# Performance work log

Hardware: AMD Instinct MI355X
Metric: run time of the kernel (lower is better)

## Reference

```python
import jax, jax.numpy as jnp
import numpy as np


def l2norm(x):
    return x / jnp.linalg.norm(x, axis=-1, keepdims=True)


def setup_inputs() -> dict:
    key = jax.random.key(0)
    ks = jax.random.split(key, 20)
    B, D, Wd, V, N, L = 384, 1024, 300, 30000, 8000, 16
    s = 1.0 / np.sqrt(D)
    inp = {
        "r": jax.random.normal(ks[0], (B, D), jnp.float32),
        "m": jax.random.normal(ks[1], (B, D), jnp.float32),
        "t": jax.random.normal(ks[2], (B, D), jnp.float32),
        "noun_token_id": jax.random.randint(ks[3], (B, L), 0, V, jnp.int32),
        "noun_len": jax.random.randint(ks[4], (B,), 1, L + 1, jnp.int32),
        "all_nouns_token": jax.random.randint(ks[5], (N,), 0, V, jnp.int32),
        "embed_table": jax.random.normal(ks[6], (V, Wd), jnp.float32) * 0.02,
        "noun_W": jax.random.normal(ks[7], (Wd, D), jnp.float32) / np.sqrt(Wd),
        "noun_b": jnp.zeros((D,), jnp.float32),
        "em_W1": jax.random.normal(ks[8], (D, D), jnp.float32) * s,
        "em_b1": jnp.zeros((D,), jnp.float32),
        "em_W2": jax.random.normal(ks[9], (D, D), jnp.float32) * s,
        "em_b2": jnp.zeros((D,), jnp.float32),
        "tr_W": jax.random.normal(ks[10], (D, D), jnp.float32) * s,
        "tr_b": jnp.zeros((D,), jnp.float32),
    }
    # dict noun_token_id_to_idx as dense map; 0 == missing (torch `if weight_idx:` falsy)
    idx = jax.random.randint(ks[11], (V,), 0, N, jnp.int32)
    present = jax.random.uniform(ks[12], (V,)) < 0.7
    inp["token_to_idx_map"] = jnp.where(present, idx, 0).astype(jnp.int32)
    return inp


def reference(r, m, t, noun_token_id, noun_len, all_nouns_token, token_to_idx_map,
              embed_table, noun_W, noun_b, em_W1, em_b1, em_W2, em_b2, tr_W, tr_b):
    B, D = m.shape
    L = noun_token_id.shape[1]

    # cls_weights = noun_encoder(embed(all_nouns_token))  -> [N, D]
    cls_weights = embed_table[all_nouns_token] @ noun_W + noun_b

    # gen_cpt: vectorized replacement of the per-token python double loop (@no_grad)
    widx = token_to_idx_map[noun_token_id]                # [B, L]
    found = widx > 0                                      # `if weight_idx:` semantics
    mapped = cls_weights[widx]                            # [B, L, D]
    fallback = embed_table[noun_token_id] @ noun_W + noun_b  # noun_encoder(embed(key))
    valid = jnp.arange(L)[None, :] < noun_len[:, None]    # [B, L]
    concepts = jnp.where((found & valid)[..., None], mapped,
                         jnp.where(valid[..., None], fallback, 0.0))
    concepts = jax.lax.stop_gradient(concepts)            # torch.no_grad

    # Attention_EM(m): Linear -> ReLU -> Linear -> Softmax(dim=1)
    h = jax.nn.relu(m @ em_W1 + em_b1)
    A_EM = jax.nn.softmax(h @ em_W2 + em_b2, axis=1)      # [B, D]
    Tr_m = l2norm(m @ tr_W + tr_b)                        # Transform_m

    # EM broadcast: (Tr_m[b] * l2norm(A_EM[b]*t[c])).sum(-1)
    # = ((Tr_m*A_EM)[b] . t[c]) / ||A_EM[b]*t[c]||, expressed as two GEMMs
    num = jnp.einsum('bd,cd->bc', Tr_m * A_EM, t)
    den = jnp.sqrt(jnp.einsum('bd,cd->bc', A_EM * A_EM, t * t))
    EM_score = num / den                                  # [B, B]

    # IS broadcast: cosine(r, t)
    IS_score = l2norm(r) @ l2norm(t).T                    # [B, B]

    score = EM_score + IS_score
    return score, concepts
```

## Files before the change

### kernel.cpp

```cpp
#include <hip/hip_runtime.h>
#include <hip/hip_bf16.h>

#define BDIM 384
#define DDIM 1024
#define LDIM 16
#define WD 300
#define CK 320
#define NROWS (BDIM * LDIM)
#define FELEM (BDIM * DDIM)
#define SELEM (BDIM * BDIM)

typedef __attribute__((ext_vector_type(8))) short short8v;
typedef _Float16 half8 __attribute__((ext_vector_type(8)));
typedef __attribute__((ext_vector_type(4))) float f32x4;

__device__ inline ushort f2bf(float x) {
    union { float f; unsigned u; } c; c.f = x;
    unsigned u = c.u;
    unsigned r = (u + 0x7fffu + ((u >> 16) & 1u)) >> 16;
    return (ushort)r;
}

#define PRE_A 1920
#define PRE_B (PRE_A + 320)
#define PRE_T (PRE_B + 3072)
#define PRE_M (PRE_T + 384)
__global__ __launch_bounds__(256) void prep_all(
    const float* __restrict__ embed, const int* __restrict__ ntid,
    const int* __restrict__ nlen, const int* __restrict__ ant, const int* __restrict__ t2i,
    ushort* __restrict__ Abf, int* __restrict__ rowtok,
    const float* __restrict__ nW, ushort* __restrict__ BbfT,
    const float* __restrict__ W1, const float* __restrict__ W2, const float* __restrict__ W3,
    _Float16* __restrict__ WT1, _Float16* __restrict__ WT2, _Float16* __restrict__ WT3,
    const float* __restrict__ m, _Float16* __restrict__ mh) {
    __shared__ float tile[32][33];
    const int b = blockIdx.x, t = threadIdx.x;

    if (b < PRE_A) {
        int idx = b * 256 + t;
        int row = idx / (CK / 4);
        int q = idx - row * (CK / 4);
        int tok = ntid[row];
        int w = t2i[tok];
        int eff = (w > 0) ? ant[w] : tok;
        bool valid = (row & 15) < nlen[row >> 4];
        if (q == 0) rowtok[row] = valid ? eff : -1;
        ushort4 o = {0, 0, 0, 0};
        if (valid && q < WD / 4) {
            float4 v = *(const float4*)&embed[(size_t)eff * WD + q * 4];
            o.x = f2bf(v.x); o.y = f2bf(v.y); o.z = f2bf(v.z); o.w = f2bf(v.w);
        }
        *(ushort4*)&Abf[(size_t)row * CK + q * 4] = o;
        return;
    }
    if (b < PRE_B) {
        int bb = b - PRE_A;
        const int k0 = (bb % 10) * 32, c0 = (bb / 10) * 32;
        const int r = t >> 3, q = t & 7;
        int k = k0 + r;
        float4 v = {0, 0, 0, 0};
        if (k < WD) v = *(const float4*)&nW[(size_t)k * DDIM + c0 + q * 4];
        tile[r][q * 4 + 0] = v.x; tile[r][q * 4 + 1] = v.y;
        tile[r][q * 4 + 2] = v.z; tile[r][q * 4 + 3] = v.w;
        __syncthreads();
        ushort4 o;
        o.x = f2bf(tile[q * 4 + 0][r]);
        o.y = f2bf(tile[q * 4 + 1][r]);
        o.z = f2bf(tile[q * 4 + 2][r]);
        o.w = f2bf(tile[q * 4 + 3][r]);
        *(ushort4*)&BbfT[(size_t)(c0 + r) * CK + k0 + q * 4] = o;
        return;
    }
    if (b < PRE_T) {
        int bb = b - PRE_B;
        int z = bb >> 10, rem = bb & 1023;
        const float* W = (z == 0) ? W1 : (z == 1) ? W2 : W3;
        _Float16* WT = (z == 0) ? WT1 : (z == 1) ? WT2 : WT3;
        const int k0 = (rem & 31) * 32, c0 = (rem >> 5) * 32;
        const int r = t >> 3, q = t & 7;
        float4 v = *(const float4*)&W[(size_t)(k0 + r) * DDIM + c0 + q * 4];
        tile[r][q * 4 + 0] = v.x; tile[r][q * 4 + 1] = v.y;
        tile[r][q * 4 + 2] = v.z; tile[r][q * 4 + 3] = v.w;
        __syncthreads();
        union { _Float16 h[4]; ushort4 u; } o;
        o.h[0] = (_Float16)tile[q * 4 + 0][r];
        o.h[1] = (_Float16)tile[q * 4 + 1][r];
        o.h[2] = (_Float16)tile[q * 4 + 2][r];
        o.h[3] = (_Float16)tile[q * 4 + 3][r];
        *(ushort4*)&WT[(size_t)(c0 + r) * DDIM + k0 + q * 4] = o.u;
        return;
    }
    {
        int bb = b - PRE_T;
        int i = bb * 1024 + t * 4;
        float4 v = *(const float4*)&m[i];
        union { _Float16 h[4]; ushort4 u; } o;
        o.h[0] = (_Float16)v.x; o.h[1] = (_Float16)v.y;
        o.h[2] = (_Float16)v.z; o.h[3] = (_Float16)v.w;
        *(ushort4*)&mh[i] = o.u;
    }
}

__global__ __launch_bounds__(256) void concepts_mfma(const ushort* __restrict__ Abf,
                                                     const ushort* __restrict__ BbfT,
                                                     const int* __restrict__ rowtok,
                                                     const float* __restrict__ bias,
                                                     float* __restrict__ C) {
    union SMem {
        struct { ushort As[2][128 * 40]; ushort Bs[2][128 * 40]; } g;
        float cst[2][128 * 68];
    };
    __shared__ __align__(16) SMem sm;
    __shared__ int stok[128];

    const int tid = threadIdx.x;
    const int bm = blockIdx.x * 128, bn = blockIdx.y * 128;
    if (tid < 128) stok[tid] = rowtok[bm + tid];

    const int w = tid >> 6, lane = tid & 63;
    const int wrow = (w & 1) * 64, wcol = (w >> 1) * 64;
    const int frow = lane & 15, fk = lane >> 4;
    const int srow = tid >> 2, spart = tid & 3;

    f32x4 acc[4][4];
#pragma unroll
    for (int i = 0; i < 4; ++i)
#pragma unroll
        for (int j = 0; j < 4; ++j) acc[i][j] = (f32x4){0.f, 0.f, 0.f, 0.f};

    int4 pa0, pa1, pb0, pb1;
    constexpr int NK = CK / 32;

#define C_LOAD(ks)                                                                   \
    {                                                                                \
        const int k0_ = (ks) * 32;                                                   \
        pa0 = *(const int4*)&Abf[(size_t)(bm + srow) * CK + k0_ + spart * 8];        \
        pa1 = *(const int4*)&Abf[(size_t)(bm + 64 + srow) * CK + k0_ + spart * 8];   \
        pb0 = *(const int4*)&BbfT[(size_t)(bn + srow) * CK + k0_ + spart * 8];       \
        pb1 = *(const int4*)&BbfT[(size_t)(bn + 64 + srow) * CK + k0_ + spart * 8];  \
    }
#define C_STORE(buf)                                                                 \
    {                                                                                \
        *(int4*)&sm.g.As[buf][srow * 40 + spart * 8] = pa0;                          \
        *(int4*)&sm.g.As[buf][(64 + srow) * 40 + spart * 8] = pa1;                   \
        *(int4*)&sm.g.Bs[buf][srow * 40 + spart * 8] = pb0;                          \
        *(int4*)&sm.g.Bs[buf][(64 + srow) * 40 + spart * 8] = pb1;                   \
    }

    C_LOAD(0);
    C_STORE(0);
    __syncthreads();
    int cur = 0;

    for (int ks = 0; ks < NK; ++ks) {
        if (ks + 1 < NK) C_LOAD(ks + 1);
        short8v a[4], b[4];
#pragma unroll
        for (int i = 0; i < 4; ++i)
            a[i] = *(const short8v*)&sm.g.As[cur][(wrow + i * 16 + frow) * 40 + fk * 8];
#pragma unroll
        for (int j = 0; j < 4; ++j)
            b[j] = *(const short8v*)&sm.g.Bs[cur][(wcol + j * 16 + frow) * 40 + fk * 8];
#pragma unroll
        for (int i = 0; i < 4; ++i)
#pragma unroll
            for (int j = 0; j < 4; ++j)
                acc[i][j] = __builtin_amdgcn_mfma_f32_16x16x32_bf16(a[i], b[j], acc[i][j], 0, 0, 0);
        if (ks + 1 < NK) C_STORE(cur ^ 1);
        __syncthreads();
        cur ^= 1;
    }
#undef C_LOAD
#undef C_STORE

    const int half = w >> 1;
#pragma unroll
    for (int i = 0; i < 4; ++i)
#pragma unroll
        for (int j = 0; j < 4; ++j)
#pragma unroll
            for (int r2 = 0; r2 < 4; ++r2) {
                int row = wrow + i * 16 + fk * 4 + r2;
                int col = j * 16 + frow;
                sm.cst[half][row * 68 + col] = acc[i][j][r2];
            }
    __syncthreads();

#pragma unroll
    for (int it = 0; it < 16; ++it) {
        int f = it * 256 + tid;
        int seg = f & 15;
        int rowh = f >> 4;
        int h2 = rowh >> 7, row = rowh & 127;
        float4 o = *(const float4*)&sm.cst[h2][row * 68 + seg * 4];
        int colb = h2 * 64 + seg * 4;
        float4 bv = *(const float4*)&bias[bn + colb];
        bool zero = (stok[row] < 0);
        o.x = zero ? 0.f : o.x + bv.x;
        o.y = zero ? 0.f : o.y + bv.y;
        o.z = zero ? 0.f : o.z + bv.z;
        o.w = zero ? 0.f : o.w + bv.w;
        *(float4*)&C[(size_t)(bm + row) * DDIM + bn + colb] = o;
    }
}

template <int MODE>
__device__ __forceinline__ void emgemm_body(const _Float16* __restrict__ Ah,
                                            const _Float16* __restrict__ WT,
                                            const float* __restrict__ bias,
                                            float* __restrict__ outF,
                                            _Float16* __restrict__ outH) {
    __shared__ __align__(16) _Float16 As[2][32 * 72];
    __shared__ __align__(16) _Float16 Bs[2][32 * 72];
    const int tid = threadIdx.x;
    const int bm = blockIdx.x * 32, bn = blockIdx.y * 32;
    const int lane = tid & 63;
    const int wrow = (tid >> 6) * 16;
    const int frow = lane & 15, fk = lane >> 4;
    const int srow = tid >> 2, spart = tid & 3;

    f32x4 acc0 = {0.f, 0.f, 0.f, 0.f}, acc1 = {0.f, 0.f, 0.f, 0.f};
    int4 pa0, pa1, pb0, pb1;
    constexpr int NK = DDIM / 64;

#define E_LOAD(ks)                                                                  \
    {                                                                               \
        const int k0_ = (ks) * 64 + spart * 16;                                     \
        pa0 = *(const int4*)&Ah[(size_t)(bm + srow) * DDIM + k0_];                  \
        pa1 = *(const int4*)&Ah[(size_t)(bm + srow) * DDIM + k0_ + 8];              \
        pb0 = *(const int4*)&WT[(size_t)(bn + srow) * DDIM + k0_];                  \
        pb1 = *(const int4*)&WT[(size_t)(bn + srow) * DDIM + k0_ + 8];              \
    }
#define E_STORE(buf)                                                                \
    {                                                                               \
        *(int4*)&As[buf][srow * 72 + spart * 16] = pa0;                             \
        *(int4*)&As[buf][srow * 72 + spart * 16 + 8] = pa1;                         \
        *(int4*)&Bs[buf][srow * 72 + spart * 16] = pb0;                             \
        *(int4*)&Bs[buf][srow * 72 + spart * 16 + 8] = pb1;                         \
    }

    E_LOAD(0);
    E_STORE(0);
    __syncthreads();
    int cur = 0;

    for (int ks = 0; ks < NK; ++ks) {
        if (ks + 1 < NK) E_LOAD(ks + 1);
#pragma unroll
        for (int kk = 0; kk < 2; ++kk) {
            half8 a = *(const half8*)&As[cur][(wrow + frow) * 72 + kk * 32 + fk * 8];
            half8 b0 = *(const half8*)&Bs[cur][frow * 72 + kk * 32 + fk * 8];
            half8 b1 = *(const half8*)&Bs[cur][(16 + frow) * 72 + kk * 32 + fk * 8];
            acc0 = __builtin_amdgcn_mfma_f32_16x16x32_f16(a, b0, acc0, 0, 0, 0);
            acc1 = __builtin_amdgcn_mfma_f32_16x16x32_f16(a, b1, acc1, 0, 0, 0);
        }
        if (ks + 1 < NK) E_STORE(cur ^ 1);
        __syncthreads();
        cur ^= 1;
    }
#undef E_LOAD
#undef E_STORE

    const int orow0 = bm + wrow + fk * 4;
    const int c0 = bn + frow, c1 = bn + 16 + frow;
    const float b0v = bias[c0], b1v = bias[c1];
#pragma unroll
    for (int r = 0; r < 4; ++r) {
        int row = orow0 + r;
        float v0 = acc0[r] + b0v;
        float v1 = acc1[r] + b1v;
        if (MODE == 1) {
            outH[(size_t)row * DDIM + c0] = (_Float16)fmaxf(v0, 0.f);
            outH[(size_t)row * DDIM + c1] = (_Float16)fmaxf(v1, 0.f);
        } else {
            outF[(size_t)row * DDIM + c0] = v0;
            outF[(size_t)row * DDIM + c1] = v1;
        }
    }
}

__global__ __launch_bounds__(128) void emgemm13(const _Float16* __restrict__ mh,
                                                const _Float16* __restrict__ WT1,
                                                const _Float16* __restrict__ WT3,
                                                const float* __restrict__ b1,
                                                const float* __restrict__ b3,
                                                _Float16* __restrict__ hh,
                                                float* __restrict__ Tr) {
    if (blockIdx.z == 0)
        emgemm_body<1>(mh, WT1, b1, nullptr, hh);
    else
        emgemm_body<0>(mh, WT3, b3, Tr, nullptr);
}

__global__ __launch_bounds__(128) void emgemm2(const _Float16* __restrict__ hh,
                                               const _Float16* __restrict__ WT2,
                                               const float* __restrict__ b2,
                                               float* __restrict__ S2) {
    emgemm_body<0>(hh, WT2, b2, S2, nullptr);
}

__device__ inline float bred_sum(float x, float* sbuf) {
#pragma unroll
    for (int off = 32; off; off >>= 1) x += __shfl_down(x, off);
    __syncthreads();
    if ((threadIdx.x & 63) == 0) sbuf[threadIdx.x >> 6] = x;
    __syncthreads();
    return sbuf[0] + sbuf[1] + sbuf[2] + sbuf[3];
}
__device__ inline float bred_max(float x, float* sbuf) {
#pragma unroll
    for (int off = 32; off; off >>= 1) x = fmaxf(x, __shfl_down(x, off));
    __syncthreads();
    if ((threadIdx.x & 63) == 0) sbuf[threadIdx.x >> 6] = x;
    __syncthreads();
    return fmaxf(fmaxf(sbuf[0], sbuf[1]), fmaxf(sbuf[2], sbuf[3]));
}

__global__ __launch_bounds__(256) void rowops(const float* __restrict__ S2,
                                              const float* __restrict__ Tr,
                                              const float* __restrict__ rr,
                                              const float* __restrict__ tt,
                                              _Float16* __restrict__ uh, _Float16* __restrict__ vh,
                                              _Float16* __restrict__ rh, _Float16* __restrict__ th,
                                              _Float16* __restrict__ t2h,
                                              float* __restrict__ inv_r,
                                              float* __restrict__ inv_t) {
    __shared__ float sbuf[4];
    const int b = blockIdx.x, tid = threadIdx.x;
    const size_t base = (size_t)b * DDIM + tid * 4;

    const float4 s4 = *(const float4*)&S2[base];
    float mx = fmaxf(fmaxf(s4.x, s4.y), fmaxf(s4.z, s4.w));
    mx = bred_max(mx, sbuf);
    float e0 = expf(s4.x - mx), e1 = expf(s4.y - mx), e2 = expf(s4.z - mx), e3 = expf(s4.w - mx);
    float sum = bred_sum(e0 + e1 + e2 + e3, sbuf);
    float invsum = 1.f / sum;

    const float4 tr4 = *(const float4*)&Tr[base];
    float ss = tr4.x * tr4.x + tr4.y * tr4.y + tr4.z * tr4.z + tr4.w * tr4.w;
    ss = bred_sum(ss, sbuf);
    float invn = 1.f / sqrtf(ss);

    float a0 = e0 * invsum, a1 = e1 * invsum, a2 = e2 * invsum, a3 = e3 * invsum;
    union { _Float16 h[4]; ushort4 u; } o;

    o.h[0] = (_Float16)(tr4.x * invn * a0 * 1024.f);
    o.h[1] = (_Float16)(tr4.y * invn * a1 * 1024.f);
    o.h[2] = (_Float16)(tr4.z * invn * a2 * 1024.f);
    o.h[3] = (_Float16)(tr4.w * invn * a3 * 1024.f);
    *(ushort4*)&uh[base] = o.u;

    float q0 = a0 * 32.f, q1 = a1 * 32.f, q2 = a2 * 32.f, q3 = a3 * 32.f;
    o.h[0] = (_Float16)(q0 * q0); o.h[1] = (_Float16)(q1 * q1);
    o.h[2] = (_Float16)(q2 * q2); o.h[3] = (_Float16)(q3 * q3);
    *(ushort4*)&vh[base] = o.u;

    const float4 r4 = *(const float4*)&rr[base];
    o.h[0] = (_Float16)r4.x; o.h[1] = (_Float16)r4.y;
    o.h[2] = (_Float16)r4.z; o.h[3] = (_Float16)r4.w;
    *(ushort4*)&rh[base] = o.u;

    const float4 t4 = *(const float4*)&tt[base];
    o.h[0] = (_Float16)t4.x; o.h[1] = (_Float16)t4.y;
    o.h[2] = (_Float16)t4.z; o.h[3] = (_Float16)t4.w;
    *(ushort4*)&th[base] = o.u;

    o.h[0] = (_Float16)(t4.x * t4.x); o.h[1] = (_Float16)(t4.y * t4.y);
    o.h[2] = (_Float16)(t4.z * t4.z); o.h[3] = (_Float16)(t4.w * t4.w);
    *(ushort4*)&t2h[base] = o.u;

    float sr = bred_sum(r4.x * r4.x + r4.y * r4.y + r4.z * r4.z + r4.w * r4.w, sbuf);
    float st = bred_sum(t4.x * t4.x + t4.y * t4.y + t4.z * t4.z + t4.w * t4.w, sbuf);
    if (tid == 0) {
        inv_r[b] = 1.f / sqrtf(sr);
        inv_t[b] = 1.f / sqrtf(st);
    }
}

__global__ __launch_bounds__(128) void score_mfma(const _Float16* __restrict__ uh,
                                                  const _Float16* __restrict__ vh,
                                                  const _Float16* __restrict__ rh,
                                                  const _Float16* __restrict__ th,
                                                  const _Float16* __restrict__ t2h,
                                                  const float* __restrict__ inv_r,
                                                  const float* __restrict__ inv_t,
                                                  float* __restrict__ out) {
    __shared__ __align__(16) _Float16 Us[2][32 * 72];
    __shared__ __align__(16) _Float16 Vs[2][32 * 72];
    __shared__ __align__(16) _Float16 Rs[2][32 * 72];
    __shared__ __align__(16) _Float16 Ts[2][32 * 72];
    __shared__ __align__(16) _Float16 Qs[2][32 * 72];

    const int tid = threadIdx.x;
    const int bm = blockIdx.x * 32, bn = blockIdx.y * 32;
    const int lane = tid & 63;
    const int wrow = (tid >> 6) * 16;
    const int frow = lane & 15, fk = lane >> 4;
    const int srow = tid >> 2, spart = tid & 3;

    f32x4 an0 = {0.f, 0.f, 0.f, 0.f}, an1 = an0;
    f32x4 ad0 = an0, ad1 = an0, ai0 = an0, ai1 = an0;
    int4 pu0, pu1, pv0, pv1, pr0, pr1, pt0, pt1, pq0, pq1;
    constexpr int NK = DDIM / 64;

#define S_LOAD(ks)                                                                   \
    {                                                                                \
        const size_t mo = (size_t)(bm + srow) * DDIM + (ks) * 64 + spart * 16;       \
        const size_t no = (size_t)(bn + srow) * DDIM + (ks) * 64 + spart * 16;       \
        pu0 = *(const int4*)&uh[mo];  pu1 = *(const int4*)&uh[mo + 8];               \
        pv0 = *(const int4*)&vh[mo];  pv1 = *(const int4*)&vh[mo + 8];               \
        pr0 = *(const int4*)&rh[mo];  pr1 = *(const int4*)&rh[mo + 8];               \
        pt0 = *(const int4*)&th[no];  pt1 = *(const int4*)&th[no + 8];               \
        pq0 = *(const int4*)&t2h[no]; pq1 = *(const int4*)&t2h[no + 8];              \
    }
#define S_STORE(buf)                                                                 \
    {                                                                                \
        const int lo = srow * 72 + spart * 16;                                       \
        *(int4*)&Us[buf][lo] = pu0; *(int4*)&Us[buf][lo + 8] = pu1;                  \
        *(int4*)&Vs[buf][lo] = pv0; *(int4*)&Vs[buf][lo + 8] = pv1;                  \
        *(int4*)&Rs[buf][lo] = pr0; *(int4*)&Rs[buf][lo + 8] = pr1;                  \
        *(int4*)&Ts[buf][lo] = pt0; *(int4*)&Ts[buf][lo + 8] = pt1;                  \
        *(int4*)&Qs[buf][lo] = pq0; *(int4*)&Qs[buf][lo + 8] = pq1;                  \
    }

    S_LOAD(0);
    S_STORE(0);
    __syncthreads();
    int cur = 0;

    for (int ks = 0; ks < NK; ++ks) {
        if (ks + 1 < NK) S_LOAD(ks + 1);
#pragma unroll
        for (int kk = 0; kk < 2; ++kk) {
            const int ao = (wrow + frow) * 72 + kk * 32 + fk * 8;
            const int bo0 = frow * 72 + kk * 32 + fk * 8;
            const int bo1 = (16 + frow) * 72 + kk * 32 + fk * 8;
            half8 au = *(const half8*)&Us[cur][ao];
            half8 av = *(const half8*)&Vs[cur][ao];
            half8 ar = *(const half8*)&Rs[cur][ao];
            half8 bt0 = *(const half8*)&Ts[cur][bo0];
            half8 bt1 = *(const half8*)&Ts[cur][bo1];
            half8 bq0 = *(const half8*)&Qs[cur][bo0];
            half8 bq1 = *(const half8*)&Qs[cur][bo1];
            an0 = __builtin_amdgcn_mfma_f32_16x16x32_f16(au, bt0, an0, 0, 0, 0);
            an1 = __builtin_amdgcn_mfma_f32_16x16x32_f16(au, bt1, an1, 0, 0, 0);
            ad0 = __builtin_amdgcn_mfma_f32_16x16x32_f16(av, bq0, ad0, 0, 0, 0);
            ad1 = __builtin_amdgcn_mfma_f32_16x16x32_f16(av, bq1, ad1, 0, 0, 0);
            ai0 = __builtin_amdgcn_mfma_f32_16x16x32_f16(ar, bt0, ai0, 0, 0, 0);
            ai1 = __builtin_amdgcn_mfma_f32_16x16x32_f16(ar, bt1, ai1, 0, 0, 0);
        }
        if (ks + 1 < NK) S_STORE(cur ^ 1);
        __syncthreads();
        cur ^= 1;
    }
#undef S_LOAD
#undef S_STORE

    const int orow0 = bm + wrow + fk * 4;
    const int c0 = bn + frow, c1 = bn + 16 + frow;
    const float it0 = inv_t[c0], it1 = inv_t[c1];
#pragma unroll
    for (int r = 0; r < 4; ++r) {
        int row = orow0 + r;
        float ir = inv_r[row];
        float em0 = an0[r] / (32.f * sqrtf(ad0[r]));
        float em1 = an1[r] / (32.f * sqrtf(ad1[r]));
        out[(size_t)row * BDIM + c0] = em0 + ai0[r] * ir * it0;
        out[(size_t)row * BDIM + c1] = em1 + ai1[r] * ir * it1;
    }
}

extern "C" void kernel_launch(void* const* d_in, const int* in_sizes, int n_in, void* d_out,
                              int out_size, void* d_ws, size_t ws_size, hipStream_t stream) {
    const float* r = (const float*)d_in[0];
    const float* m = (const float*)d_in[1];
    const float* t = (const float*)d_in[2];
    const int* ntid = (const int*)d_in[3];
    const int* nlen = (const int*)d_in[4];
    const int* ant = (const int*)d_in[5];
    const float* embed = (const float*)d_in[6];
    const float* noun_W = (const float*)d_in[7];
    const float* noun_b = (const float*)d_in[8];
    const float* em_W1 = (const float*)d_in[9];
    const float* em_b1 = (const float*)d_in[10];
    const float* em_W2 = (const float*)d_in[11];
    const float* em_b2 = (const float*)d_in[12];
    const float* tr_W = (const float*)d_in[13];
    const float* tr_b = (const float*)d_in[14];
    const int* t2i = (const int*)d_in[15];

    float* score = (float*)d_out;
    float* concepts = score + (size_t)SELEM;

    char* base = (char*)d_ws;
    size_t off = 0;
    auto alloc = [&](size_t bytes) { char* p = base + off; off += (bytes + 255) & ~(size_t)255; return p; };
    int* rowtok = (int*)alloc(NROWS * 4);
    float* inv_r = (float*)alloc(BDIM * 4);
    float* inv_t = (float*)alloc(BDIM * 4);
    ushort* Abf = (ushort*)alloc((size_t)NROWS * CK * 2);
    ushort* BbfT = (ushort*)alloc((size_t)DDIM * CK * 2);
    _Float16* WT1 = (_Float16*)alloc((size_t)DDIM * DDIM * 2);
    _Float16* WT2 = (_Float16*)alloc((size_t)DDIM * DDIM * 2);
    _Float16* WT3 = (_Float16*)alloc((size_t)DDIM * DDIM * 2);
    _Float16* mh = (_Float16*)alloc((size_t)FELEM * 2);
    _Float16* hh = (_Float16*)alloc((size_t)FELEM * 2);
    float* S2 = (float*)alloc((size_t)FELEM * 4);
    float* Tr = (float*)alloc((size_t)FELEM * 4);
    _Float16* uh = (_Float16*)alloc((size_t)FELEM * 2);
    _Float16* vh = (_Float16*)alloc((size_t)FELEM * 2);
    _Float16* rh = (_Float16*)alloc((size_t)FELEM * 2);
    _Float16* th = (_Float16*)alloc((size_t)FELEM * 2);
    _Float16* t2h = (_Float16*)alloc((size_t)FELEM * 2);

    prep_all<<<PRE_M, 256, 0, stream>>>(embed, ntid, nlen, ant, t2i, Abf, rowtok,
                                        noun_W, BbfT, em_W1, em_W2, tr_W, WT1, WT2, WT3,
                                        m, mh);

    dim3 gC(NROWS / 128, DDIM / 128);
    concepts_mfma<<<gC, 256, 0, stream>>>(Abf, BbfT, rowtok, noun_b, concepts);

    dim3 g13(BDIM / 32, DDIM / 32, 2);
    emgemm13<<<g13, 128, 0, stream>>>(mh, WT1, WT3, em_b1, tr_b, hh, Tr);

    dim3 gG(BDIM / 32, DDIM / 32);
    emgemm2<<<gG, 128, 0, stream>>>(hh, WT2, em_b2, S2);

    rowops<<<BDIM, 256, 0, stream>>>(S2, Tr, r, t, uh, vh, rh, th, t2h, inv_r, inv_t);

    dim3 gS(BDIM / 32, BDIM / 32);
    score_mfma<<<gS, 128, 0, stream>>>(uh, vh, rh, th, t2h, inv_r, inv_t, score);
}
```

Before: 59.39 us.

## Fuse tail GEMMs, rowops and score into one persistent kernel with grid barriers

Replaces the four tail launches (EM GEMM1/3, GEMM2, row softmax/normalisation, score GEMM) with a single persistent kernel that strides over work units and separates phases with an atomic-counter grid barrier. Rowops is rewritten for 128-thread blocks, and shared memory is unioned across phases. The aim is to remove kernel launch gaps and tail drain between dependent stages. In exchange it adds barrier spin cost, makes correctness depend on every block being co-resident (sized from an occupancy query, but launched normally rather than cooperatively), and adds host-side attribute queries on every call.

```diff
diff --git a/kernel.cpp b/kernel.cpp
--- a/kernel.cpp
+++ b/kernel.cpp
@@ -204,16 +204,49 @@
     }
 }
 
+struct TailArgs {
+    const _Float16 *mh, *WT1, *WT2, *WT3;
+    const float *b1, *b2, *b3;
+    _Float16 *hh;
+    float *S2, *Tr;
+    const float *rr, *tt;
+    _Float16 *uh, *vh, *rh, *th, *t2h;
+    float *inv_r, *inv_t, *out;
+};
+
+union TailSMem {
+    struct { _Float16 As[2][32 * 72]; _Float16 Bs[2][32 * 72]; } e;
+    struct { _Float16 U[2][32 * 72], V[2][32 * 72], R[2][32 * 72],
+             T[2][32 * 72], Q[2][32 * 72]; } s;
+    float sb[2];
+};
+
+__device__ __forceinline__ float bsum128(float x, float* sb) {
+#pragma unroll
+    for (int off = 32; off; off >>= 1) x += __shfl_down(x, off);
+    __syncthreads();
+    if ((threadIdx.x & 63) == 0) sb[threadIdx.x >> 6] = x;
+    __syncthreads();
+    return sb[0] + sb[1];
+}
+__device__ __forceinline__ float bmax128(float x, float* sb) {
+#pragma unroll
+    for (int off = 32; off; off >>= 1) x = fmaxf(x, __shfl_down(x, off));
+    __syncthreads();
+    if ((threadIdx.x & 63) == 0) sb[threadIdx.x >> 6] = x;
+    __syncthreads();
+    return fmaxf(sb[0], sb[1]);
+}
+
 template <int MODE>
 __device__ __forceinline__ void emgemm_body(const _Float16* __restrict__ Ah,
                                             const _Float16* __restrict__ WT,
                                             const float* __restrict__ bias,
                                             float* __restrict__ outF,
-                                            _Float16* __restrict__ outH) {
-    __shared__ __align__(16) _Float16 As[2][32 * 72];
-    __shared__ __align__(16) _Float16 Bs[2][32 * 72];
+                                            _Float16* __restrict__ outH,
+                                            int bm, int bn,
+                                            _Float16 (*As)[2304], _Float16 (*Bs)[2304]) {
     const int tid = threadIdx.x;
-    const int bm = blockIdx.x * 32, bn = blockIdx.y * 32;
     const int lane = tid & 63;
     const int wrow = (tid >> 6) * 16;
     const int frow = lane & 15, fk = lane >> 4;
@@ -279,120 +312,91 @@
     }
 }
 
-__global__ __launch_bounds__(128) void emgemm13(const _Float16* __restrict__ mh,
-                                                const _Float16* __restrict__ WT1,
-                                                const _Float16* __restrict__ WT3,
-                                                const float* __restrict__ b1,
-                                                const float* __restrict__ b3,
-                                                _Float16* __restrict__ hh,
-                                                float* __restrict__ Tr) {
-    if (blockIdx.z == 0)
-        emgemm_body<1>(mh, WT1, b1, nullptr, hh);
-    else
-        emgemm_body<0>(mh, WT3, b3, Tr, nullptr);
-}
-
-__global__ __launch_bounds__(128) void emgemm2(const _Float16* __restrict__ hh,
-                                               const _Float16* __restrict__ WT2,
-                                               const float* __restrict__ b2,
-                                               float* __restrict__ S2) {
-    emgemm_body<0>(hh, WT2, b2, S2, nullptr);
-}
-
-__device__ inline float bred_sum(float x, float* sbuf) {
-#pragma unroll
-    for (int off = 32; off; off >>= 1) x += __shfl_down(x, off);
-    __syncthreads();
-    if ((threadIdx.x & 63) == 0) sbuf[threadIdx.x >> 6] = x;
-    __syncthreads();
-    return sbuf[0] + sbuf[1] + sbuf[2] + sbuf[3];
-}
-__device__ inline float bred_max(float x, float* sbuf) {
-#pragma unroll
-    for (int off = 32; off; off >>= 1) x = fmaxf(x, __shfl_down(x, off));
-    __syncthreads();
-    if ((threadIdx.x & 63) == 0) sbuf[threadIdx.x >> 6] = x;
-    __syncthreads();
-    return fmaxf(fmaxf(sbuf[0], sbuf[1]), fmaxf(sbuf[2], sbuf[3]));
-}
-
-__global__ __launch_bounds__(256) void rowops(const float* __restrict__ S2,
-                                              const float* __restrict__ Tr,
-                                              const float* __restrict__ rr,
-                                              const float* __restrict__ tt,
-                                              _Float16* __restrict__ uh, _Float16* __restrict__ vh,
-                                              _Float16* __restrict__ rh, _Float16* __restrict__ th,
-                                              _Float16* __restrict__ t2h,
-                                              float* __restrict__ inv_r,
-                                              float* __restrict__ inv_t) {
-    __shared__ float sbuf[4];
-    const int b = blockIdx.x, tid = threadIdx.x;
-    const size_t base = (size_t)b * DDIM + tid * 4;
-
-    const float4 s4 = *(const float4*)&S2[base];
-    float mx = fmaxf(fmaxf(s4.x, s4.y), fmaxf(s4.z, s4.w));
-    mx = bred_max(mx, sbuf);
-    float e0 = expf(s4.x - mx), e1 = expf(s4.y - mx), e2 = expf(s4.z - mx), e3 = expf(s4.w - mx);
-    float sum = bred_sum(e0 + e1 + e2 + e3, sbuf);
+__device__ __forceinline__ void rowops_body(const TailArgs& a, float* sb, int b) {
+    const int tid = threadIdx.x;
+    const size_t base = (size_t)b * DDIM;
+    const int cA = tid * 4, cB = 512 + tid * 4;
+
+    float4 sA = *(const float4*)&a.S2[base + cA];
+    float4 sB = *(const float4*)&a.S2[base + cB];
+    float mx = fmaxf(fmaxf(fmaxf(sA.x, sA.y), fmaxf(sA.z, sA.w)),
+                     fmaxf(fmaxf(sB.x, sB.y), fmaxf(sB.z, sB.w)));
+    mx = bmax128(mx, sb);
+    float eA0 = expf(sA.x - mx), eA1 = expf(sA.y - mx), eA2 = expf(sA.z - mx), eA3 = expf(sA.w - mx);
+    float eB0 = expf(sB.x - mx), eB1 = expf(sB.y - mx), eB2 = expf(sB.z - mx), eB3 = expf(sB.w - mx);
+    float sum = bsum128(eA0 + eA1 + eA2 + eA3 + eB0 + eB1 + eB2 + eB3, sb);
     float invsum = 1.f / sum;
 
-    const float4 tr4 = *(const float4*)&Tr[base];
-    float ss = tr4.x * tr4.x + tr4.y * tr4.y + tr4.z * tr4.z + tr4.w * tr4.w;
-    ss = bred_sum(ss, sbuf);
+    float4 trA = *(const float4*)&a.Tr[base + cA];
+    float4 trB = *(const float4*)&a.Tr[base + cB];
+    float ss = trA.x * trA.x + trA.y * trA.y + trA.z * trA.z + trA.w * trA.w +
+               trB.x * trB.x + trB.y * trB.y + trB.z * trB.z + trB.w * trB.w;
+    ss = bsum128(ss, sb);
     float invn = 1.f / sqrtf(ss);
 
-    float a0 = e0 * invsum, a1 = e1 * invsum, a2 = e2 * invsum, a3 = e3 * invsum;
+    float aA0 = eA0 * invsum, aA1 = eA1 * invsum, aA2 = eA2 * invsum, aA3 = eA3 * invsum;
+    float aB0 = eB0 * invsum, aB1 = eB1 * invsum, aB2 = eB2 * invsum, aB3 = eB3 * invsum;
     union { _Float16 h[4]; ushort4 u; } o;
 
-    o.h[0] = (_Float16)(tr4.x * invn * a0 * 1024.f);
-    o.h[1] = (_Float16)(tr4.y * invn * a1 * 1024.f);
-    o.h[2] = (_Float16)(tr4.z * invn * a2 * 1024.f);
-    o.h[3] = (_Float16)(tr4.w * invn * a3 * 1024.f);
-    *(ushort4*)&uh[base] = o.u;
-
-    float q0 = a0 * 32.f, q1 = a1 * 32.f, q2 = a2 * 32.f, q3 = a3 * 32.f;
-    o.h[0] = (_Float16)(q0 * q0); o.h[1] = (_Float16)(q1 * q1);
-    o.h[2] = (_Float16)(q2 * q2); o.h[3] = (_Float16)(q3 * q3);
-    *(ushort4*)&vh[base] = o.u;
-
-    const float4 r4 = *(const float4*)&rr[base];
-    o.h[0] = (_Float16)r4.x; o.h[1] = (_Float16)r4.y;
-    o.h[2] = (_Float16)r4.z; o.h[3] = (_Float16)r4.w;
-    *(ushort4*)&rh[base] = o.u;
-
-    const float4 t4 = *(const float4*)&tt[base];
-    o.h[0] = (_Float16)t4.x; o.h[1] = (_Float16)t4.y;
-    o.h[2] = (_Float16)t4.z; o.h[3] = (_Float16)t4.w;
-    *(ushort4*)&th[base] = o.u;
-
-    o.h[0] = (_Float16)(t4.x * t4.x); o.h[1] = (_Float16)(t4.y * t4.y);
-    o.h[2] = (_Float16)(t4.z * t4.z); o.h[3] = (_Float16)(t4.w * t4.w);
-    *(ushort4*)&t2h[base] = o.u;
-
-    float sr = bred_sum(r4.x * r4.x + r4.y * r4.y + r4.z * r4.z + r4.w * r4.w, sbuf);
-    float st = bred_sum(t4.x * t4.x + t4.y * t4.y + t4.z * t4.z + t4.w * t4.w, sbuf);
+    o.h[0] = (_Float16)(trA.x * invn * aA0 * 1024.f);
+    o.h[1] = (_Float16)(trA.y * invn * aA1 * 1024.f);
+    o.h[2] = (_Float16)(trA.z * invn * aA2 * 1024.f);
+    o.h[3] = (_Float16)(trA.w * invn * aA3 * 1024.f);
+    *(ushort4*)&a.uh[base + cA] = o.u;
+    o.h[0] = (_Float16)(trB.x * invn * aB0 * 1024.f);
+    o.h[1] = (_Float16)(trB.y * invn * aB1 * 1024.f);
+    o.h[2] = (_Float16)(trB.z * invn * aB2 * 1024.f);
+    o.h[3] = (_Float16)(trB.w * invn * aB3 * 1024.f);
+    *(ushort4*)&a.uh[base + cB] = o.u;
+
+    float qA0 = aA0 * 32.f, qA1 = aA1 * 32.f, qA2 = aA2 * 32.f, qA3 = aA3 * 32.f;
+    float qB0 = aB0 * 32.f, qB1 = aB1 * 32.f, qB2 = aB2 * 32.f, qB3 = aB3 * 32.f;
+    o.h[0] = (_Float16)(qA0 * qA0); o.h[1] = (_Float16)(qA1 * qA1);
+    o.h[2] = (_Float16)(qA2 * qA2); o.h[3] = (_Float16)(qA3 * qA3);
+    *(ushort4*)&a.vh[base + cA] = o.u;
+    o.h[0] = (_Float16)(qB0 * qB0); o.h[1] = (_Float16)(qB1 * qB1);
+    o.h[2] = (_Float16)(qB2 * qB2); o.h[3] = (_Float16)(qB3 * qB3);
+    *(ushort4*)&a.vh[base + cB] = o.u;
+
+    float4 rA = *(const float4*)&a.rr[base + cA];
+    float4 rB = *(const float4*)&a.rr[base + cB];
+    o.h[0] = (_Float16)rA.x; o.h[1] = (_Float16)rA.y;
+    o.h[2] = (_Float16)rA.z; o.h[3] = (_Float16)rA.w;
+    *(ushort4*)&a.rh[base + cA] = o.u;
+    o.h[0] = (_Float16)rB.x; o.h[1] = (_Float16)rB.y;
+    o.h[2] = (_Float16)rB.z; o.h[3] = (_Float16)rB.w;
+    *(ushort4*)&a.rh[base + cB] = o.u;
+    float sr = bsum128(rA.x * rA.x + rA.y * rA.y + rA.z * rA.z + rA.w * rA.w +
+                       rB.x * rB.x + rB.y * rB.y + rB.z * rB.z + rB.w * rB.w, sb);
+
+    float4 tA = *(const float4*)&a.tt[base + cA];
+    float4 tB = *(const float4*)&a.tt[base + cB];
+    o.h[0] = (_Float16)tA.x; o.h[1] = (_Float16)tA.y;
+    o.h[2] = (_Float16)tA.z; o.h[3] = (_Float16)tA.w;
+    *(ushort4*)&a.th[base + cA] = o.u;
+    o.h[0] = (_Float16)tB.x; o.h[1] = (_Float16)tB.y;
+    o.h[2] = (_Float16)tB.z; o.h[3] = (_Float16)tB.w;
+    *(ushort4*)&a.th[base + cB] = o.u;
+    o.h[0] = (_Float16)(tA.x * tA.x); o.h[1] = (_Float16)(tA.y * tA.y);
+    o.h[2] = (_Float16)(tA.z * tA.z); o.h[3] = (_Float16)(tA.w * tA.w);
+    *(ushort4*)&a.t2h[base + cA] = o.u;
+    o.h[0] = (_Float16)(tB.x * tB.x); o.h[1] = (_Float16)(tB.y * tB.y);
+    o.h[2] = (_Float16)(tB.z * tB.z); o.h[3] = (_Float16)(tB.w * tB.w);
+    *(ushort4*)&a.t2h[base + cB] = o.u;
+    float st = bsum128(tA.x * tA.x + tA.y * tA.y + tA.z * tA.z + tA.w * tA.w +
+                       tB.x * tB.x + tB.y * tB.y + tB.z * tB.z + tB.w * tB.w, sb);
+
     if (tid == 0) {
-        inv_r[b] = 1.f / sqrtf(sr);
-        inv_t[b] = 1.f / sqrtf(st);
-    }
-}
-
-__global__ __launch_bounds__(128) void score_mfma(const _Float16* __restrict__ uh,
-                                                  const _Float16* __restrict__ vh,
-                                                  const _Float16* __restrict__ rh,
-                                                  const _Float16* __restrict__ th,
-                                                  const _Float16* __restrict__ t2h,
-                                                  const float* __restrict__ inv_r,
-                                                  const float* __restrict__ inv_t,
-                                                  float* __restrict__ out) {
-    __shared__ __align__(16) _Float16 Us[2][32 * 72];
-    __shared__ __align__(16) _Float16 Vs[2][32 * 72];
-    __shared__ __align__(16) _Float16 Rs[2][32 * 72];
-    __shared__ __align__(16) _Float16 Ts[2][32 * 72];
-    __shared__ __align__(16) _Float16 Qs[2][32 * 72];
+        a.inv_r[b] = 1.f / sqrtf(sr);
+        a.inv_t[b] = 1.f / sqrtf(st);
+    }
+}
+
+__device__ __forceinline__ void score_body(const TailArgs& a, TailSMem* sm, int bm, int bn) {
+    auto Us = sm->s.U; auto Vs = sm->s.V; auto Rs = sm->s.R;
+    auto Ts = sm->s.T; auto Qs = sm->s.Q;
 
     const int tid = threadIdx.x;
-    const int bm = blockIdx.x * 32, bn = blockIdx.y * 32;
     const int lane = tid & 63;
     const int wrow = (tid >> 6) * 16;
     const int frow = lane & 15, fk = lane >> 4;
@@ -407,11 +411,11 @@
     {                                                                                \
         const size_t mo = (size_t)(bm + srow) * DDIM + (ks) * 64 + spart * 16;       \
         const size_t no = (size_t)(bn + srow) * DDIM + (ks) * 64 + spart * 16;       \
-        pu0 = *(const int4*)&uh[mo];  pu1 = *(const int4*)&uh[mo + 8];               \
-        pv0 = *(const int4*)&vh[mo];  pv1 = *(const int4*)&vh[mo + 8];               \
-        pr0 = *(const int4*)&rh[mo];  pr1 = *(const int4*)&rh[mo + 8];               \
-        pt0 = *(const int4*)&th[no];  pt1 = *(const int4*)&th[no + 8];               \
-        pq0 = *(const int4*)&t2h[no]; pq1 = *(const int4*)&t2h[no + 8];              \
+        pu0 = *(const int4*)&a.uh[mo];  pu1 = *(const int4*)&a.uh[mo + 8];           \
+        pv0 = *(const int4*)&a.vh[mo];  pv1 = *(const int4*)&a.vh[mo + 8];           \
+        pr0 = *(const int4*)&a.rh[mo];  pr1 = *(const int4*)&a.rh[mo + 8];           \
+        pt0 = *(const int4*)&a.th[no];  pt1 = *(const int4*)&a.th[no + 8];           \
+        pq0 = *(const int4*)&a.t2h[no]; pq1 = *(const int4*)&a.t2h[no + 8];          \
     }
 #define S_STORE(buf)                                                                 \
     {                                                                                \
@@ -458,16 +462,64 @@
 
     const int orow0 = bm + wrow + fk * 4;
     const int c0 = bn + frow, c1 = bn + 16 + frow;
-    const float it0 = inv_t[c0], it1 = inv_t[c1];
+    const float it0 = a.inv_t[c0], it1 = a.inv_t[c1];
 #pragma unroll
     for (int r = 0; r < 4; ++r) {
         int row = orow0 + r;
-        float ir = inv_r[row];
+        float ir = a.inv_r[row];
         float em0 = an0[r] / (32.f * sqrtf(ad0[r]));
         float em1 = an1[r] / (32.f * sqrtf(ad1[r]));
-        out[(size_t)row * BDIM + c0] = em0 + ai0[r] * ir * it0;
-        out[(size_t)row * BDIM + c1] = em1 + ai1[r] * ir * it1;
-    }
+        a.out[(size_t)row * BDIM + c0] = em0 + ai0[r] * ir * it0;
+        a.out[(size_t)row * BDIM + c1] = em1 + ai1[r] * ir * it1;
+    }
+}
+
+__device__ __forceinline__ void run_unit(const TailArgs& a, TailSMem* sm, int phase, int u) {
+    if (phase == 0) {
+        int v = (u < 384) ? u : u - 384;
+        int bm = (v % 12) * 32, bn = (v / 12) * 32;
+        if (u < 384)
+            emgemm_body<1>(a.mh, a.WT1, a.b1, nullptr, a.hh, bm, bn, sm->e.As, sm->e.Bs);
+        else
+            emgemm_body<0>(a.mh, a.WT3, a.b3, a.Tr, nullptr, bm, bn, sm->e.As, sm->e.Bs);
+    } else if (phase == 1) {
+        int bm = (u % 12) * 32, bn = (u / 12) * 32;
+        emgemm_body<0>(a.hh, a.WT2, a.b2, a.S2, nullptr, bm, bn, sm->e.As, sm->e.Bs);
+    } else if (phase == 2) {
+        rowops_body(a, sm->sb, u);
+    } else {
+        int bm = (u % 12) * 32, bn = (u / 12) * 32;
+        score_body(a, sm, bm, bn);
+    }
+}
+
+__device__ __forceinline__ void grid_bar(unsigned* cnt, unsigned target) {
+    __syncthreads();
+    if (threadIdx.x == 0) {
+        __threadfence();
+        atomicAdd(cnt, 1u);
+        while (__hip_atomic_load(cnt, __ATOMIC_RELAXED, __HIP_MEMORY_SCOPE_AGENT) < target)
+            __builtin_amdgcn_s_sleep(8);
+        __threadfence();
+    }
+    __syncthreads();
+}
+
+__global__ __launch_bounds__(128) void coop_tail(TailArgs a, unsigned* cnt) {
+    __shared__ TailSMem sm;
+    const unsigned bid = blockIdx.x, G = gridDim.x;
+    for (unsigned u = bid; u < 768; u += G) run_unit(a, &sm, 0, u);
+    grid_bar(cnt, G);
+    for (unsigned u = bid; u < 384; u += G) run_unit(a, &sm, 1, u);
+    grid_bar(cnt, 2 * G);
+    for (unsigned u = bid; u < 384; u += G) run_unit(a, &sm, 2, u);
+    grid_bar(cnt, 3 * G);
+    for (unsigned u = bid; u < 144; u += G) run_unit(a, &sm, 3, u);
+}
+
+__global__ __launch_bounds__(128) void tail_k(TailArgs a, int phase) {
+    __shared__ TailSMem sm;
+    run_unit(a, &sm, phase, blockIdx.x);
 }
 
 extern "C" void kernel_launch(void* const* d_in, const int* in_sizes, int n_in, void* d_out,
@@ -495,6 +547,7 @@
     char* base = (char*)d_ws;
     size_t off = 0;
     auto alloc = [&](size_t bytes) { char* p = base + off; off += (bytes + 255) & ~(size_t)255; return p; };
+    unsigned* cnt = (unsigned*)alloc(256);
     int* rowtok = (int*)alloc(NROWS * 4);
     float* inv_r = (float*)alloc(BDIM * 4);
     float* inv_t = (float*)alloc(BDIM * 4);
@@ -513,6 +566,8 @@
     _Float16* th = (_Float16*)alloc((size_t)FELEM * 2);
     _Float16* t2h = (_Float16*)alloc((size_t)FELEM * 2);
 
+    hipMemsetAsync(cnt, 0, sizeof(unsigned), stream);
+
     prep_all<<<PRE_M, 256, 0, stream>>>(embed, ntid, nlen, ant, t2i, Abf, rowtok,
                                         noun_W, BbfT, em_W1, em_W2, tr_W, WT1, WT2, WT3,
                                         m, mh);
@@ -520,14 +575,31 @@
     dim3 gC(NROWS / 128, DDIM / 128);
     concepts_mfma<<<gC, 256, 0, stream>>>(Abf, BbfT, rowtok, noun_b, concepts);
 
-    dim3 g13(BDIM / 32, DDIM / 32, 2);
-    emgemm13<<<g13, 128, 0, stream>>>(mh, WT1, WT3, em_b1, tr_b, hh, Tr);
-
-    dim3 gG(BDIM / 32, DDIM / 32);
-    emgemm2<<<gG, 128, 0, stream>>>(hh, WT2, em_b2, S2);
-
-    rowops<<<BDIM, 256, 0, stream>>>(S2, Tr, r, t, uh, vh, rh, th, t2h, inv_r, inv_t);
-
-    dim3 gS(BDIM / 32, BDIM / 32);
-    score_mfma<<<gS, 128, 0, stream>>>(uh, vh, rh, th, t2h, inv_r, inv_t, score);
-}
+    TailArgs ta;
+    ta.mh = mh; ta.WT1 = WT1; ta.WT2 = WT2; ta.WT3 = WT3;
+    ta.b1 = em_b1; ta.b2 = em_b2; ta.b3 = tr_b;
+    ta.hh = hh; ta.S2 = S2; ta.Tr = Tr;
+    ta.rr = r; ta.tt = t;
+    ta.uh = uh; ta.vh = vh; ta.rh = rh; ta.th = th; ta.t2h = t2h;
+    ta.inv_r = inv_r; ta.inv_t = inv_t; ta.out = score;
+
+    int dev = 0;
+    (void)hipGetDevice(&dev);
+    int cus = 0;
+    (void)hipDeviceGetAttribute(&cus, hipDeviceAttributeMultiprocessorCount, dev);
+    int nb = 0;
+    hipError_t qe = hipOccupancyMaxActiveBlocksPerMultiprocessor(
+        &nb, reinterpret_cast<const void*>(coop_tail), 128, 0);
+
+    long G = (qe == hipSuccess && nb > 0 && cus > 0) ? (long)nb * cus : 0;
+    if (G > 768) G = 768;
+
+    if (G >= 64) {
+        coop_tail<<<dim3((unsigned)G), 128, 0, stream>>>(ta, cnt);
+    } else {
+        tail_k<<<768, 128, 0, stream>>>(ta, 0);
+        tail_k<<<384, 128, 0, stream>>>(ta, 1);
+        tail_k<<<384, 128, 0, stream>>>(ta, 2);
+        tail_k<<<144, 128, 0, stream>>>(ta, 3);
+    }
+}
```

After: 210.1 us. 3.54x slower.

## Merge concepts GEMM and EM first-layer GEMMs into one launch with 256-thread EM tiles

Applied to the files above, without the earlier changes.

Folds the concepts GEMM and the two independent EM first-stage GEMMs (W1 and tr_W) into a single kernel that dispatches on block index, so they run concurrently and a launch is removed. The EM GEMM body is reworked to use 256 threads per 32x32 tile, with each wave computing one 16x16 sub-tile instead of 128 threads computing two. This gives more waves per tile and better occupancy for these small GEMMs. In exchange, the EM blocks in the fused kernel reserve the large shared-memory footprint sized for the concepts tile, which may limit how many blocks fit per CU.

```diff
diff --git a/kernel.cpp b/kernel.cpp
--- a/kernel.cpp
+++ b/kernel.cpp
@@ -101,20 +101,105 @@
     }
 }
 
-__global__ __launch_bounds__(256) void concepts_mfma(const ushort* __restrict__ Abf,
-                                                     const ushort* __restrict__ BbfT,
-                                                     const int* __restrict__ rowtok,
-                                                     const float* __restrict__ bias,
-                                                     float* __restrict__ C) {
-    union SMem {
-        struct { ushort As[2][128 * 40]; ushort Bs[2][128 * 40]; } g;
-        float cst[2][128 * 68];
-    };
-    __shared__ __align__(16) SMem sm;
-    __shared__ int stok[128];
-
+template <int MODE>
+__device__ __forceinline__ void emgemm_body256(const _Float16* __restrict__ Ah,
+                                               const _Float16* __restrict__ WT,
+                                               const float* __restrict__ bias,
+                                               float* __restrict__ outF,
+                                               _Float16* __restrict__ outH,
+                                               int bm, int bn,
+                                               _Float16* As, _Float16* Bs) {
     const int tid = threadIdx.x;
-    const int bm = blockIdx.x * 128, bn = blockIdx.y * 128;
+    const int lane = tid & 63;
+    const int w = tid >> 6;
+    const int hr = (w & 1) * 16, hc = (w >> 1) * 16;
+    const int frow = lane & 15, fk = lane >> 4;
+    const int srow = tid >> 3, spart = tid & 7;
+
+    f32x4 acc = {0.f, 0.f, 0.f, 0.f};
+    int4 pa, pb;
+    constexpr int NK = DDIM / 64;
+
+#define E_LOAD(ks)                                                                  \
+    {                                                                               \
+        const int k0_ = (ks) * 64 + spart * 8;                                      \
+        pa = *(const int4*)&Ah[(size_t)(bm + srow) * DDIM + k0_];                   \
+        pb = *(const int4*)&WT[(size_t)(bn + srow) * DDIM + k0_];                   \
+    }
+#define E_STORE(buf)                                                                \
+    {                                                                               \
+        *(int4*)&As[(buf) * 2304 + srow * 72 + spart * 8] = pa;                     \
+        *(int4*)&Bs[(buf) * 2304 + srow * 72 + spart * 8] = pb;                     \
+    }
+
+    E_LOAD(0);
+    E_STORE(0);
+    __syncthreads();
+    int cur = 0;
+
+    for (int ks = 0; ks < NK; ++ks) {
+        if (ks + 1 < NK) E_LOAD(ks + 1);
+#pragma unroll
+        for (int kk = 0; kk < 2; ++kk) {
+            half8 a = *(const half8*)&As[cur * 2304 + (hr + frow) * 72 + kk * 32 + fk * 8];
+            half8 b = *(const half8*)&Bs[cur * 2304 + (hc + frow) * 72 + kk * 32 + fk * 8];
+            acc = __builtin_amdgcn_mfma_f32_16x16x32_f16(a, b, acc, 0, 0, 0);
+        }
+        if (ks + 1 < NK) E_STORE(cur ^ 1);
+        __syncthreads();
+        cur ^= 1;
+    }
+#undef E_LOAD
+#undef E_STORE
+
+    const int col = bn + hc + frow;
+    const float bv = bias[col];
+#pragma unroll
+    for (int r2 = 0; r2 < 4; ++r2) {
+        int row = bm + hr + fk * 4 + r2;
+        float v = acc[r2] + bv;
+        if (MODE == 1)
+            outH[(size_t)row * DDIM + col] = (_Float16)fmaxf(v, 0.f);
+        else
+            outF[(size_t)row * DDIM + col] = v;
+    }
+}
+
+__global__ __launch_bounds__(256) void mega2(const ushort* __restrict__ Abf,
+                                             const ushort* __restrict__ BbfT,
+                                             const int* __restrict__ rowtok,
+                                             const float* __restrict__ nbias,
+                                             float* __restrict__ C,
+                                             const _Float16* __restrict__ mh,
+                                             const _Float16* __restrict__ WT1,
+                                             const _Float16* __restrict__ WT3,
+                                             const float* __restrict__ b1,
+                                             const float* __restrict__ b3,
+                                             _Float16* __restrict__ hh,
+                                             float* __restrict__ Tr) {
+    __shared__ __align__(16) char smem[69632 + 512];
+    const int blk = blockIdx.x;
+    const int tid = threadIdx.x;
+
+    if (blk >= 384) {
+        int u = blk - 384;
+        int v = (u < 384) ? u : u - 384;
+        int bm = (v % 12) * 32, bn = (v / 12) * 32;
+        _Float16* As = (_Float16*)smem;
+        _Float16* Bs = (_Float16*)(smem + 9216);
+        if (u < 384)
+            emgemm_body256<1>(mh, WT1, b1, nullptr, hh, bm, bn, As, Bs);
+        else
+            emgemm_body256<0>(mh, WT3, b3, Tr, nullptr, bm, bn, As, Bs);
+        return;
+    }
+
+    ushort* CAs = (ushort*)smem;
+    ushort* CBs = (ushort*)(smem + 20480);
+    float*  cst = (float*)smem;
+    int* stok = (int*)(smem + 69632);
+
+    const int bm = (blk % 48) * 128, bn = (blk / 48) * 128;
     if (tid < 128) stok[tid] = rowtok[bm + tid];
 
     const int w = tid >> 6, lane = tid & 63;
@@ -141,10 +226,10 @@
     }
 #define C_STORE(buf)                                                                 \
     {                                                                                \
-        *(int4*)&sm.g.As[buf][srow * 40 + spart * 8] = pa0;                          \
-        *(int4*)&sm.g.As[buf][(64 + srow) * 40 + spart * 8] = pa1;                   \
-        *(int4*)&sm.g.Bs[buf][srow * 40 + spart * 8] = pb0;                          \
-        *(int4*)&sm.g.Bs[buf][(64 + srow) * 40 + spart * 8] = pb1;                   \
+        *(int4*)&CAs[(buf) * 5120 + srow * 40 + spart * 8] = pa0;                    \
+        *(int4*)&CAs[(buf) * 5120 + (64 + srow) * 40 + spart * 8] = pa1;             \
+        *(int4*)&CBs[(buf) * 5120 + srow * 40 + spart * 8] = pb0;                    \
+        *(int4*)&CBs[(buf) * 5120 + (64 + srow) * 40 + spart * 8] = pb1;             \
     }
 
     C_LOAD(0);
@@ -157,10 +242,10 @@
         short8v a[4], b[4];
 #pragma unroll
         for (int i = 0; i < 4; ++i)
-            a[i] = *(const short8v*)&sm.g.As[cur][(wrow + i * 16 + frow) * 40 + fk * 8];
+            a[i] = *(const short8v*)&CAs[cur * 5120 + (wrow + i * 16 + frow) * 40 + fk * 8];
 #pragma unroll
         for (int j = 0; j < 4; ++j)
-            b[j] = *(const short8v*)&sm.g.Bs[cur][(wcol + j * 16 + frow) * 40 + fk * 8];
+            b[j] = *(const short8v*)&CBs[cur * 5120 + (wcol + j * 16 + frow) * 40 + fk * 8];
 #pragma unroll
         for (int i = 0; i < 4; ++i)
 #pragma unroll
@@ -182,7 +267,7 @@
             for (int r2 = 0; r2 < 4; ++r2) {
                 int row = wrow + i * 16 + fk * 4 + r2;
                 int col = j * 16 + frow;
-                sm.cst[half][row * 68 + col] = acc[i][j][r2];
+                cst[half * 8704 + row * 68 + col] = acc[i][j][r2];
             }
     __syncthreads();
 
@@ -192,9 +277,9 @@
         int seg = f & 15;
         int rowh = f >> 4;
         int h2 = rowh >> 7, row = rowh & 127;
-        float4 o = *(const float4*)&sm.cst[h2][row * 68 + seg * 4];
+        float4 o = *(const float4*)&cst[h2 * 8704 + row * 68 + seg * 4];
         int colb = h2 * 64 + seg * 4;
-        float4 bv = *(const float4*)&bias[bn + colb];
+        float4 bv = *(const float4*)&nbias[bn + colb];
         bool zero = (stok[row] < 0);
         o.x = zero ? 0.f : o.x + bv.x;
         o.y = zero ? 0.f : o.y + bv.y;
@@ -204,99 +289,15 @@
     }
 }
 
-template <int MODE>
-__device__ __forceinline__ void emgemm_body(const _Float16* __restrict__ Ah,
-                                            const _Float16* __restrict__ WT,
-                                            const float* __restrict__ bias,
-                                            float* __restrict__ outF,
-                                            _Float16* __restrict__ outH) {
-    __shared__ __align__(16) _Float16 As[2][32 * 72];
-    __shared__ __align__(16) _Float16 Bs[2][32 * 72];
-    const int tid = threadIdx.x;
-    const int bm = blockIdx.x * 32, bn = blockIdx.y * 32;
-    const int lane = tid & 63;
-    const int wrow = (tid >> 6) * 16;
-    const int frow = lane & 15, fk = lane >> 4;
-    const int srow = tid >> 2, spart = tid & 3;
-
-    f32x4 acc0 = {0.f, 0.f, 0.f, 0.f}, acc1 = {0.f, 0.f, 0.f, 0.f};
-    int4 pa0, pa1, pb0, pb1;
-    constexpr int NK = DDIM / 64;
-
-#define E_LOAD(ks)                                                                  \
-    {                                                                               \
-        const int k0_ = (ks) * 64 + spart * 16;                                     \
-        pa0 = *(const int4*)&Ah[(size_t)(bm + srow) * DDIM + k0_];                  \
-        pa1 = *(const int4*)&Ah[(size_t)(bm + srow) * DDIM + k0_ + 8];              \
-        pb0 = *(const int4*)&WT[(size_t)(bn + srow) * DDIM + k0_];                  \
-        pb1 = *(const int4*)&WT[(size_t)(bn + srow) * DDIM + k0_ + 8];              \
-    }
-#define E_STORE(buf)                                                                \
-    {                                                                               \
-        *(int4*)&As[buf][srow * 72 + spart * 16] = pa0;                             \
-        *(int4*)&As[buf][srow * 72 + spart * 16 + 8] = pa1;                         \
-        *(int4*)&Bs[buf][srow * 72 + spart * 16] = pb0;                             \
-        *(int4*)&Bs[buf][srow * 72 + spart * 16 + 8] = pb1;                         \
-    }
-
-    E_LOAD(0);
-    E_STORE(0);
-    __syncthreads();
-    int cur = 0;
-
-    for (int ks = 0; ks < NK; ++ks) {
-        if (ks + 1 < NK) E_LOAD(ks + 1);
-#pragma unroll
-        for (int kk = 0; kk < 2; ++kk) {
-            half8 a = *(const half8*)&As[cur][(wrow + frow) * 72 + kk * 32 + fk * 8];
-            half8 b0 = *(const half8*)&Bs[cur][frow * 72 + kk * 32 + fk * 8];
-            half8 b1 = *(const half8*)&Bs[cur][(16 + frow) * 72 + kk * 32 + fk * 8];
-            acc0 = __builtin_amdgcn_mfma_f32_16x16x32_f16(a, b0, acc0, 0, 0, 0);
-            acc1 = __builtin_amdgcn_mfma_f32_16x16x32_f16(a, b1, acc1, 0, 0, 0);
-        }
-        if (ks + 1 < NK) E_STORE(cur ^ 1);
-        __syncthreads();
-        cur ^= 1;
-    }
-#undef E_LOAD
-#undef E_STORE
-
-    const int orow0 = bm + wrow + fk * 4;
-    const int c0 = bn + frow, c1 = bn + 16 + frow;
-    const float b0v = bias[c0], b1v = bias[c1];
-#pragma unroll
-    for (int r = 0; r < 4; ++r) {
-        int row = orow0 + r;
-        float v0 = acc0[r] + b0v;
-        float v1 = acc1[r] + b1v;
-        if (MODE == 1) {
-            outH[(size_t)row * DDIM + c0] = (_Float16)fmaxf(v0, 0.f);
-            outH[(size_t)row * DDIM + c1] = (_Float16)fmaxf(v1, 0.f);
-        } else {
-            outF[(size_t)row * DDIM + c0] = v0;
-            outF[(size_t)row * DDIM + c1] = v1;
-        }
-    }
-}
-
-__global__ __launch_bounds__(128) void emgemm13(const _Float16* __restrict__ mh,
-                                                const _Float16* __restrict__ WT1,
-                                                const _Float16* __restrict__ WT3,
-                                                const float* __restrict__ b1,
-                                                const float* __restrict__ b3,
-                                                _Float16* __restrict__ hh,
-                                                float* __restrict__ Tr) {
-    if (blockIdx.z == 0)
-        emgemm_body<1>(mh, WT1, b1, nullptr, hh);
-    else
-        emgemm_body<0>(mh, WT3, b3, Tr, nullptr);
-}
-
-__global__ __launch_bounds__(128) void emgemm2(const _Float16* __restrict__ hh,
-                                               const _Float16* __restrict__ WT2,
-                                               const float* __restrict__ b2,
-                                               float* __restrict__ S2) {
-    emgemm_body<0>(hh, WT2, b2, S2, nullptr);
+__global__ __launch_bounds__(256) void em2k(const _Float16* __restrict__ hh,
+                                            const _Float16* __restrict__ WT2,
+                                            const float* __restrict__ b2,
+                                            float* __restrict__ S2) {
+    __shared__ __align__(16) _Float16 As[2 * 2304];
+    __shared__ __align__(16) _Float16 Bs[2 * 2304];
+    int u = blockIdx.x;
+    int bm = (u % 12) * 32, bn = (u / 12) * 32;
+    emgemm_body256<0>(hh, WT2, b2, S2, nullptr, bm, bn, As, Bs);
 }
 
 __device__ inline float bred_sum(float x, float* sbuf) {
@@ -517,14 +518,10 @@
                                         noun_W, BbfT, em_W1, em_W2, tr_W, WT1, WT2, WT3,
                                         m, mh);
 
-    dim3 gC(NROWS / 128, DDIM / 128);
-    concepts_mfma<<<gC, 256, 0, stream>>>(Abf, BbfT, rowtok, noun_b, concepts);
-
-    dim3 g13(BDIM / 32, DDIM / 32, 2);
-    emgemm13<<<g13, 128, 0, stream>>>(mh, WT1, WT3, em_b1, tr_b, hh, Tr);
-
-    dim3 gG(BDIM / 32, DDIM / 32);
-    emgemm2<<<gG, 128, 0, stream>>>(hh, WT2, em_b2, S2);
+    mega2<<<1152, 256, 0, stream>>>(Abf, BbfT, rowtok, noun_b, concepts,
+                                    mh, WT1, WT3, em_b1, tr_b, hh, Tr);
+
+    em2k<<<384, 256, 0, stream>>>(hh, WT2, em_b2, S2);
 
     rowops<<<BDIM, 256, 0, stream>>>(S2, Tr, r, t, uh, vh, rh, th, t2h, inv_r, inv_t);
 
```

Result: slower. 61.62 us (+3.8%).
